# Performance work log

Hardware: AMD Instinct MI355X
Metric: run time of the kernel (lower is better)

## Reference

```python
import jax, jax.numpy as jnp
import numpy as np

N = 100000   # nodes
E = 1000000  # edges per scale
F = 500      # num_features
H = 64       # nhid
C = 40       # num_classes
S = 3        # scales = len(d_list) - 1


def setup_inputs() -> dict:
    key = jax.random.key(0)
    ks = jax.random.split(key, 24)
    inp = {}
    inp["x"] = jax.random.normal(ks[0], (N, F), jnp.float32)
    for i in range(S):
        inp[f"edge_index_{i+1}"] = jax.random.randint(ks[1 + i], (2, E), 0, N, dtype=jnp.int32)
        inp[f"edge_attr_{i+1}"] = jax.random.uniform(ks[4 + i], (E,), jnp.float32)
    # linear1: num_features -> nhid
    inp["W1"] = jax.random.normal(ks[7], (F, H), jnp.float32) * (1.0 / np.sqrt(F))
    inp["b1"] = jnp.zeros((H,), jnp.float32)
    # UFG filters, block 1 and block 2: uniform(0.7*i, 0.7*i + 0.1), shape [1, H]
    for i in range(S):
        lo = 0.7 * (i + 1)
        inp[f"filt1_{i+1}"] = jax.random.uniform(ks[8 + i], (1, H), jnp.float32, lo, lo + 0.1)
        inp[f"filt2_{i+1}"] = jax.random.uniform(ks[11 + i], (1, H), jnp.float32, lo, lo + 0.1)
    # mlp2: Linear(3*H, H) (after ReLU+Dropout)
    inp["W_mlp2"] = jax.random.normal(ks[14], (3 * H, H), jnp.float32) * (1.0 / np.sqrt(3 * H))
    inp["b_mlp2"] = jnp.zeros((H,), jnp.float32)
    # mlp1: Linear(3*H, C)
    inp["W_mlp1"] = jax.random.normal(ks[15], (3 * H, C), jnp.float32) * (1.0 / np.sqrt(3 * H))
    inp["b_mlp1"] = jnp.zeros((C,), jnp.float32)
    return inp


def _ufg(x, edge_index, edge_attr, filt):
    # MessagePassing(aggr='add'): out[dst] = sum_e attr_e * x[src_e]; then * filter
    src, dst = edge_index[0], edge_index[1]
    msg = edge_attr[:, None] * x[src]                       # [E, H]
    agg = jax.ops.segment_sum(msg, dst, num_segments=N)     # [N, H]
    return agg * filt


def reference(x, edge_index_1, edge_attr_1, edge_index_2, edge_attr_2,
              edge_index_3, edge_attr_3, W1, b1,
              filt1_1, filt1_2, filt1_3, filt2_1, filt2_2, filt2_3,
              W_mlp2, b_mlp2, W_mlp1, b_mlp1):
    eis = (edge_index_1, edge_index_2, edge_index_3)
    eas = (edge_attr_1, edge_attr_2, edge_attr_3)
    f1 = (filt1_1, filt1_2, filt1_3)
    f2 = (filt2_1, filt2_2, filt2_3)

    h = x @ W1 + b1                                          # [N, H]
    h = jnp.concatenate([_ufg(h, ei, ea, f) for ei, ea, f in zip(eis, eas, f1)], axis=1)  # [N, 3H]
    h = jax.nn.relu(h) @ W_mlp2 + b_mlp2                     # mlp2 (dropout = identity in eval)
    h = jnp.concatenate([_ufg(h, ei, ea, f) for ei, ea, f in zip(eis, eas, f2)], axis=1)  # [N, 3H]
    h = jax.nn.relu(h) @ W_mlp1 + b_mlp1                     # mlp1
    return jax.nn.log_softmax(h, axis=1)
```

## Files before the change

### kernel.cpp

```cpp
#include <hip/hip_runtime.h>
#include <hip/hip_bf16.h>

#define NN 100000
#define FF 500
#define HH 64
#define CC 40
#define EE 1000000
#define NB 782
#define NBK 2346
#define NBLK_P 256
#define M2 (NBK * NBLK_P)

typedef __attribute__((ext_vector_type(8))) short short8v;
typedef __attribute__((ext_vector_type(4))) float f32x4;

__device__ inline unsigned relu2bf16(unsigned u)
{
    unsigned r = (u & 0x00008000u) ? (u & 0xFFFF0000u) : u;
    return (r & 0x80000000u) ? (r & 0x0000FFFFu) : r;
}

__global__ __launch_bounds__(256) void build_w1t(
    const float* __restrict__ W1, __hip_bfloat16* __restrict__ W1t)
{
    int idx = blockIdx.x * 256 + threadIdx.x;
    if (idx >= 64 * 512) return;
    int col = idx >> 9;
    int k = idx & 511;
    W1t[idx] = (k < FF) ? __float2bfloat16(W1[(size_t)k * 64 + col])
                        : __float2bfloat16(0.f);
}

__global__ __launch_bounds__(256) void build_wm2t(
    const float* __restrict__ Wm2, __hip_bfloat16* __restrict__ Wm2t)
{
    int idx = blockIdx.x * 256 + threadIdx.x;
    if (idx >= 64 * 192) return;
    int col = idx / 192;
    int k = idx - col * 192;
    Wm2t[idx] = __float2bfloat16(Wm2[(size_t)k * 64 + col]);
}

__global__ __launch_bounds__(256) void gemm1_mfma(
    const float* __restrict__ X,
    const __hip_bfloat16* __restrict__ W1t,
    const float* __restrict__ bias,
    __hip_bfloat16* __restrict__ H,
    int nrows)
{
    __shared__ __hip_bfloat16 As[64][40];
    __shared__ __hip_bfloat16 Bs[64][40];

    const int t = threadIdx.x;
    const int lane = t & 63;
    const int w = t >> 6;
    const int row0 = blockIdx.x * 64;
    const int kg = lane >> 4;
    const int lr = lane & 15;

    f32x4 acc[4] = {};

    const int arow = t >> 2;
    const int akq = (t & 3) * 8;
    const int bcol = t >> 2;
    const int bkq = (t & 3) * 8;

    int grow = row0 + arow;
    const float* xp = X + (size_t)(grow < nrows ? grow : nrows - 1) * FF;

    float va[8];
    uint4 vb;
    {
        float4 a0 = *(const float4*)(xp + akq);
        float4 a1 = *(const float4*)(xp + akq + 4);
        va[0]=a0.x; va[1]=a0.y; va[2]=a0.z; va[3]=a0.w;
        va[4]=a1.x; va[5]=a1.y; va[6]=a1.z; va[7]=a1.w;
        vb = *(const uint4*)(W1t + (size_t)bcol * 512 + bkq);
    }

    for (int k0 = 0; k0 < FF; k0 += 32) {
        {
            unsigned q[4];
            #pragma unroll
            for (int i = 0; i < 4; ++i) {
                __hip_bfloat162 pp =
                    __float22bfloat162_rn(make_float2(va[2*i], va[2*i+1]));
                q[i] = *(unsigned*)&pp;
            }
            *(uint4*)&As[arow][akq] = make_uint4(q[0], q[1], q[2], q[3]);
            *(uint4*)&Bs[bcol][bkq] = vb;
        }

        const int kn = k0 + 32;
        float va2[8];
        uint4 vb2;
        if (kn < FF) {
            if (kn + 32 <= FF) {
                float4 a0 = *(const float4*)(xp + kn + akq);
                float4 a1 = *(const float4*)(xp + kn + akq + 4);
                va2[0]=a0.x; va2[1]=a0.y; va2[2]=a0.z; va2[3]=a0.w;
                va2[4]=a1.x; va2[5]=a1.y; va2[6]=a1.z; va2[7]=a1.w;
            } else {
                #pragma unroll
                for (int j = 0; j < 8; ++j) {
                    int kk = kn + akq + j;
                    va2[j] = (kk < FF) ? xp[kk] : 0.f;
                }
            }
            vb2 = *(const uint4*)(W1t + (size_t)bcol * 512 + kn + bkq);
        }
        __syncthreads();

        short8v a0 = *(const short8v*)&As[w * 16 + lr][kg * 8];
        short8v b0 = *(const short8v*)&Bs[lr][kg * 8];
        short8v b1 = *(const short8v*)&Bs[16 + lr][kg * 8];
        short8v b2 = *(const short8v*)&Bs[32 + lr][kg * 8];
        short8v b3 = *(const short8v*)&Bs[48 + lr][kg * 8];
        acc[0] = __builtin_amdgcn_mfma_f32_16x16x32_bf16(a0, b0, acc[0], 0, 0, 0);
        acc[1] = __builtin_amdgcn_mfma_f32_16x16x32_bf16(a0, b1, acc[1], 0, 0, 0);
        acc[2] = __builtin_amdgcn_mfma_f32_16x16x32_bf16(a0, b2, acc[2], 0, 0, 0);
        acc[3] = __builtin_amdgcn_mfma_f32_16x16x32_bf16(a0, b3, acc[3], 0, 0, 0);
        __syncthreads();

        if (kn < FF) {
            #pragma unroll
            for (int j = 0; j < 8; ++j) va[j] = va2[j];
            vb = vb2;
        }
    }

    float bv[4];
    #pragma unroll
    for (int n = 0; n < 4; ++n) bv[n] = bias[n * 16 + lr];

    #pragma unroll
    for (int n = 0; n < 4; ++n) {
        #pragma unroll
        for (int r = 0; r < 4; ++r) {
            int row = row0 + w * 16 + kg * 4 + r;
            if (row < nrows)
                H[(size_t)row * 64 + n * 16 + lr] =
                    __float2bfloat16(acc[n][r] + bv[n]);
        }
    }
}

__global__ __launch_bounds__(256) void gemm2_mfma(
    const __hip_bfloat16* __restrict__ A,
    const __hip_bfloat16* __restrict__ Bt,
    const float* __restrict__ bias,
    __hip_bfloat16* __restrict__ H,
    int nrows)
{
    __shared__ __hip_bfloat16 As[128][40];
    __shared__ __hip_bfloat16 Bs[64][40];

    const int t = threadIdx.x;
    const int lane = t & 63;
    const int w = t >> 6;
    const int row0 = blockIdx.x * 128;
    const int wrow = w * 32;
    const int kg = lane >> 4;
    const int lr = lane & 15;

    f32x4 acc[2][4] = {};

    const int arow = t >> 1;
    const int akh = t & 1;
    const int bcol = t >> 2;
    const int bkq = t & 3;

    for (int k0 = 0; k0 < 192; k0 += 32) {
        {
            int grow = row0 + arow;
            int gr = grow < nrows ? grow : nrows - 1;
            const __hip_bfloat16* ap = A + (size_t)gr * 192 + k0 + akh * 16;
            uint4 u0 = *(const uint4*)ap;
            uint4 u1 = *(const uint4*)(ap + 8);
            u0.x = relu2bf16(u0.x); u0.y = relu2bf16(u0.y);
            u0.z = relu2bf16(u0.z); u0.w = relu2bf16(u0.w);
            u1.x = relu2bf16(u1.x); u1.y = relu2bf16(u1.y);
            u1.z = relu2bf16(u1.z); u1.w = relu2bf16(u1.w);
            *(uint4*)&As[arow][akh * 16]     = u0;
            *(uint4*)&As[arow][akh * 16 + 8] = u1;
        }
        *(uint4*)&Bs[bcol][bkq * 8] =
            *(const uint4*)(Bt + (size_t)bcol * 192 + k0 + bkq * 8);
        __syncthreads();

        short8v a0 = *(const short8v*)&As[wrow + lr][kg * 8];
        short8v a1 = *(const short8v*)&As[wrow + 16 + lr][kg * 8];
        short8v b0 = *(const short8v*)&Bs[lr][kg * 8];
        short8v b1 = *(const short8v*)&Bs[16 + lr][kg * 8];
        short8v b2 = *(const short8v*)&Bs[32 + lr][kg * 8];
        short8v b3 = *(const short8v*)&Bs[48 + lr][kg * 8];
        acc[0][0] = __builtin_amdgcn_mfma_f32_16x16x32_bf16(a0, b0, acc[0][0], 0, 0, 0);
        acc[0][1] = __builtin_amdgcn_mfma_f32_16x16x32_bf16(a0, b1, acc[0][1], 0, 0, 0);
        acc[0][2] = __builtin_amdgcn_mfma_f32_16x16x32_bf16(a0, b2, acc[0][2], 0, 0, 0);
        acc[0][3] = __builtin_amdgcn_mfma_f32_16x16x32_bf16(a0, b3, acc[0][3], 0, 0, 0);
        acc[1][0] = __builtin_amdgcn_mfma_f32_16x16x32_bf16(a1, b0, acc[1][0], 0, 0, 0);
        acc[1][1] = __builtin_amdgcn_mfma_f32_16x16x32_bf16(a1, b1, acc[1][1], 0, 0, 0);
        acc[1][2] = __builtin_amdgcn_mfma_f32_16x16x32_bf16(a1, b2, acc[1][2], 0, 0, 0);
        acc[1][3] = __builtin_amdgcn_mfma_f32_16x16x32_bf16(a1, b3, acc[1][3], 0, 0, 0);
        __syncthreads();
    }

    float bv[4];
    #pragma unroll
    for (int n = 0; n < 4; ++n) bv[n] = bias[n * 16 + lr];

    #pragma unroll
    for (int m = 0; m < 2; ++m) {
        #pragma unroll
        for (int n = 0; n < 4; ++n) {
            #pragma unroll
            for (int r = 0; r < 4; ++r) {
                int row = row0 + wrow + m * 16 + kg * 4 + r;
                if (row < nrows)
                    H[(size_t)row * 64 + n * 16 + lr] =
                        __float2bfloat16(acc[m][n][r] + bv[n]);
            }
        }
    }
}

__global__ __launch_bounds__(1024) void part_count(
    const int* __restrict__ ei1, const int* __restrict__ ei2,
    const int* __restrict__ ei3, int* __restrict__ cnt)
{
    __shared__ int lc[NBK];
    const int t = threadIdx.x;
    for (int j = t; j < NBK; j += 1024) lc[j] = 0;
    __syncthreads();

    const int chunk = (3 * EE + NBLK_P - 1) / NBLK_P;
    const int b0 = blockIdx.x * chunk;
    int b1 = b0 + chunk;
    if (b1 > 3 * EE) b1 = 3 * EE;

    for (int i = b0 + t; i < b1; i += 1024) {
        int s = i / EE;
        int e = i - s * EE;
        const int* ei = (s == 0) ? ei1 : (s == 1) ? ei2 : ei3;
        atomicAdd(&lc[s * NB + (ei[EE + e] >> 7)], 1);
    }
    __syncthreads();
    for (int j = t; j < NBK; j += 1024)
        cnt[j * NBLK_P + blockIdx.x] = lc[j];
}

__global__ __launch_bounds__(1024) void scan_a(
    const int* __restrict__ cnt, int* __restrict__ off,
    int* __restrict__ partials, int M)
{
    __shared__ int sh[1024];
    int t = threadIdx.x;
    int i = blockIdx.x * 1024 + t;
    int v = (i < M) ? cnt[i] : 0;
    sh[t] = v;
    __syncthreads();
    #pragma unroll
    for (int o = 1; o < 1024; o <<= 1) {
        int add = (t >= o) ? sh[t - o] : 0;
        __syncthreads();
        sh[t] += add;
        __syncthreads();
    }
    if (i < M) off[i] = sh[t] - v;
    if (t == 1023) partials[blockIdx.x] = sh[1023];
}

__global__ __launch_bounds__(1024) void scan_b(int* __restrict__ partials, int P)
{
    __shared__ int sh[1024];
    int t = threadIdx.x;
    int v = (t < P) ? partials[t] : 0;
    sh[t] = v;
    __syncthreads();
    #pragma unroll
    for (int o = 1; o < 1024; o <<= 1) {
        int add = (t >= o) ? sh[t - o] : 0;
        __syncthreads();
        sh[t] += add;
        __syncthreads();
    }
    if (t < P) partials[t] = sh[t] - v;
}

__global__ __launch_bounds__(256) void scan_c(
    int* __restrict__ off, int* __restrict__ off_b,
    const int* __restrict__ partials, int M)
{
    int i = blockIdx.x * 256 + threadIdx.x;
    if (i < M) {
        int v = off[i] + partials[i >> 10];
        off[i] = v;
        if ((i & (NBLK_P - 1)) == 0) off_b[i / NBLK_P] = v;
    }
    if (i == 0) off_b[NBK] = 3 * EE;
}

__global__ __launch_bounds__(1024) void part_scatter(
    const int* __restrict__ ei1, const float* __restrict__ ea1,
    const int* __restrict__ ei2, const float* __restrict__ ea2,
    const int* __restrict__ ei3, const float* __restrict__ ea3,
    const int* __restrict__ offp, int2* __restrict__ brec)
{
    __shared__ int lcur[NBK];
    const int t = threadIdx.x;
    for (int j = t; j < NBK; j += 1024)
        lcur[j] = offp[j * NBLK_P + blockIdx.x];
    __syncthreads();

    const int chunk = (3 * EE + NBLK_P - 1) / NBLK_P;
    const int b0 = blockIdx.x * chunk;
    int b1 = b0 + chunk;
    if (b1 > 3 * EE) b1 = 3 * EE;

    for (int i = b0 + t; i < b1; i += 1024) {
        int s = i / EE;
        int e = i - s * EE;
        const int* ei = (s == 0) ? ei1 : (s == 1) ? ei2 : ei3;
        const float* ea = (s == 0) ? ea1 : (s == 1) ? ea2 : ea3;
        int src = ei[e];
        int dst = ei[EE + e];
        float w = ea[e];
        int pos = atomicAdd(&lcur[s * NB + (dst >> 7)], 1);
        brec[pos] = make_int2(src | ((dst & 127) << 17), __float_as_int(w));
    }
}

__global__ __launch_bounds__(256) void bucket_refine(
    const int2* __restrict__ brec,
    const int* __restrict__ off_b,
    int* __restrict__ node_off,
    int2* __restrict__ pairs)
{
    __shared__ int hist[128];
    __shared__ int curls[128];
    const int t = threadIdx.x;
    const int bk = blockIdx.x;
    const int s = bk / NB;
    const int b = bk - s * NB;
    const int n0 = b << 7;
    const int beg = off_b[bk];
    const int end = off_b[bk + 1];

    if (bk == 0 && t == 0) node_off[3 * NN] = 3 * EE;
    if (t < 128) hist[t] = 0;
    __syncthreads();

    for (int p = beg + t; p < end; p += 256)
        atomicAdd(&hist[(brec[p].x >> 17) & 127], 1);
    __syncthreads();

    int cnt = (t < 128) ? hist[t] : 0;
    #pragma unroll
    for (int o = 1; o < 128; o <<= 1) {
        int add = (t < 128 && t >= o) ? hist[t - o] : 0;
        __syncthreads();
        if (t < 128) hist[t] += add;
        __syncthreads();
    }
    if (t < 128) {
        int excl = beg + hist[t] - cnt;
        curls[t] = excl;
        if (n0 + t < NN) node_off[s * NN + n0 + t] = excl;
    }
    __syncthreads();

    for (int p = beg + t; p < end; p += 256) {
        int2 r = brec[p];
        int pos = atomicAdd(&curls[(r.x >> 17) & 127], 1);
        pairs[pos] = make_int2(r.x & 0x1FFFF, r.y);
    }
}

__device__ inline void drain_seg(
    const __hip_bfloat16* __restrict__ h, const int2* __restrict__ pairs,
    unsigned lane, int p, int end, float& acc0, float& acc1)
{
    for (; p + 8 <= end; p += 8) {
        int2 q[8];
        #pragma unroll
        for (int i = 0; i < 8; ++i) q[i] = pairs[p + i];
        float v[8];
        #pragma unroll
        for (int i = 0; i < 8; ++i)
            v[i] = __bfloat162float(h[((unsigned)q[i].x << 6) | lane]);
        #pragma unroll
        for (int i = 0; i < 8; i += 2) {
            acc0 = fmaf(__int_as_float(q[i].y), v[i], acc0);
            acc1 = fmaf(__int_as_float(q[i + 1].y), v[i + 1], acc1);
        }
    }
    if (p + 4 <= end) {
        int2 q[4];
        #pragma unroll
        for (int i = 0; i < 4; ++i) q[i] = pairs[p + i];
        float v[4];
        #pragma unroll
        for (int i = 0; i < 4; ++i)
            v[i] = __bfloat162float(h[((unsigned)q[i].x << 6) | lane]);
        acc0 = fmaf(__int_as_float(q[0].y), v[0], acc0);
        acc1 = fmaf(__int_as_float(q[1].y), v[1], acc1);
        acc0 = fmaf(__int_as_float(q[2].y), v[2], acc0);
        acc1 = fmaf(__int_as_float(q[3].y), v[3], acc1);
        p += 4;
    }
    if (p + 2 <= end) {
        int2 q0 = pairs[p];
        int2 q1 = pairs[p + 1];
        float v0 = __bfloat162float(h[((unsigned)q0.x << 6) | lane]);
        float v1 = __bfloat162float(h[((unsigned)q1.x << 6) | lane]);
        acc0 = fmaf(__int_as_float(q0.y), v0, acc0);
        acc1 = fmaf(__int_as_float(q1.y), v1, acc1);
        p += 2;
    }
    if (p < end) {
        int2 q = pairs[p];
        acc0 = fmaf(__int_as_float(q.y),
                    __bfloat162float(h[((unsigned)q.x << 6) | lane]), acc0);
    }
}

__global__ __launch_bounds__(256) void ufg_gather(
    const __hip_bfloat16* __restrict__ h,
    const int* __restrict__ off,
    const int2* __restrict__ pairs,
    const float* __restrict__ f1, const float* __restrict__ f2,
    const float* __restrict__ f3,
    __hip_bfloat16* __restrict__ agg)
{
    const unsigned lane = threadIdx.x & 63;
    int wp0 = blockIdx.x * 4 + (threadIdx.x >> 6);
    const int wp = __builtin_amdgcn_readfirstlane(wp0);
    if (wp >= (3 * NN) / 2) return;
    const int segA = wp * 2;
    const int s = segA / NN;
    const int nA = segA - s * NN;

    const float* fp = (s == 0) ? f1 : (s == 1) ? f2 : f3;
    const float fv = fp[lane];

    const int begA = off[segA];
    const int endA = off[segA + 1];
    const int endB = off[segA + 2];

    float aA0 = 0.f, aA1 = 0.f, aB0 = 0.f, aB1 = 0.f;
    int pA = begA, pB = endA;

    while (pA + 8 <= endA && pB + 8 <= endB) {
        int2 qa[8], qb[8];
        #pragma unroll
        for (int i = 0; i < 8; ++i) qa[i] = pairs[pA + i];
        #pragma unroll
        for (int i = 0; i < 8; ++i) qb[i] = pairs[pB + i];
        float va[8], vb[8];
        #pragma unroll
        for (int i = 0; i < 8; ++i)
            va[i] = __bfloat162float(h[((unsigned)qa[i].x << 6) | lane]);
        #pragma unroll
        for (int i = 0; i < 8; ++i)
            vb[i] = __bfloat162float(h[((unsigned)qb[i].x << 6) | lane]);
        #pragma unroll
        for (int i = 0; i < 8; i += 2) {
            aA0 = fmaf(__int_as_float(qa[i].y), va[i], aA0);
            aA1 = fmaf(__int_as_float(qa[i + 1].y), va[i + 1], aA1);
            aB0 = fmaf(__int_as_float(qb[i].y), vb[i], aB0);
            aB1 = fmaf(__int_as_float(qb[i + 1].y), vb[i + 1], aB1);
        }
        pA += 8;
        pB += 8;
    }
    while (pA + 4 <= endA && pB + 4 <= endB) {
        int2 qa[4], qb[4];
        #pragma unroll
        for (int i = 0; i < 4; ++i) qa[i] = pairs[pA + i];
        #pragma unroll
        for (int i = 0; i < 4; ++i) qb[i] = pairs[pB + i];
        float va[4], vb[4];
        #pragma unroll
        for (int i = 0; i < 4; ++i)
            va[i] = __bfloat162float(h[((unsigned)qa[i].x << 6) | lane]);
        #pragma unroll
        for (int i = 0; i < 4; ++i)
            vb[i] = __bfloat162float(h[((unsigned)qb[i].x << 6) | lane]);
        aA0 = fmaf(__int_as_float(qa[0].y), va[0], aA0);
        aA1 = fmaf(__int_as_float(qa[1].y), va[1], aA1);
        aA0 = fmaf(__int_as_float(qa[2].y), va[2], aA0);
        aA1 = fmaf(__int_as_float(qa[3].y), va[3], aA1);
        aB0 = fmaf(__int_as_float(qb[0].y), vb[0], aB0);
        aB1 = fmaf(__int_as_float(qb[1].y), vb[1], aB1);
        aB0 = fmaf(__int_as_float(qb[2].y), vb[2], aB0);
        aB1 = fmaf(__int_as_float(qb[3].y), vb[3], aB1);
        pA += 4;
        pB += 4;
    }
    drain_seg(h, pairs, lane, pA, endA, aA0, aA1);
    drain_seg(h, pairs, lane, pB, endB, aB0, aB1);

    agg[(size_t)nA * 192 + s * 64 + lane] =
        __float2bfloat16((aA0 + aA1) * fv);
    agg[(size_t)(nA + 1) * 192 + s * 64 + lane] =
        __float2bfloat16((aB0 + aB1) * fv);
}

__global__ __launch_bounds__(256) void gemm40_softmax(
    const __hip_bfloat16* __restrict__ A,
    const float* __restrict__ B,
    const float* __restrict__ bias,
    float* __restrict__ out,
    int nrows)
{
    __shared__ float As[32][68];
    __shared__ float Bs[32][64];

    const int tid = threadIdx.x;
    const int tx = tid & 15;
    const int ty = tid >> 4;
    const int row0 = blockIdx.x * 64;

    float acc[4][4] = {{0.f, 0.f, 0.f, 0.f}, {0.f, 0.f, 0.f, 0.f},
                       {0.f, 0.f, 0.f, 0.f}, {0.f, 0.f, 0.f, 0.f}};

    const int r = tid >> 2;
    const int koff = (tid & 3) * 8;
    const bool rowok = (row0 + r) < nrows;

    for (int k0 = 0; k0 < 192; k0 += 32) {
        float av[8];
        const __hip_bfloat16* ap = A + (size_t)(row0 + r) * 192 + (k0 + koff);
        if (rowok) {
            uint4 u = *(const uint4*)ap;
            av[0] = __uint_as_float(u.x << 16);
            av[1] = __uint_as_float(u.x & 0xFFFF0000u);
            av[2] = __uint_as_float(u.y << 16);
            av[3] = __uint_as_float(u.y & 0xFFFF0000u);
            av[4] = __uint_as_float(u.z << 16);
            av[5] = __uint_as_float(u.z & 0xFFFF0000u);
            av[6] = __uint_as_float(u.w << 16);
            av[7] = __uint_as_float(u.w & 0xFFFF0000u);
        } else {
            #pragma unroll
            for (int j = 0; j < 8; ++j) av[j] = 0.f;
        }
        #pragma unroll
        for (int j = 0; j < 8; ++j) As[koff + j][r] = fmaxf(av[j], 0.f);

        {
            int flat = tid * 8;
            int kk = flat >> 6;
            int c0 = flat & 63;
            #pragma unroll
            for (int j = 0; j < 8; ++j) {
                int cc = c0 + j;
                Bs[kk][cc] = (cc < 40) ? B[(size_t)(k0 + kk) * 40 + cc] : 0.f;
            }
        }
        __syncthreads();

        #pragma unroll
        for (int k = 0; k < 32; ++k) {
            float4 a = *(const float4*)&As[k][ty * 4];
            float4 b = *(const float4*)&Bs[k][tx * 4];
            acc[0][0] = fmaf(a.x, b.x, acc[0][0]);
            acc[0][1] = fmaf(a.x, b.y, acc[0][1]);
            acc[0][2] = fmaf(a.x, b.z, acc[0][2]);
            acc[0][3] = fmaf(a.x, b.w, acc[0][3]);
            acc[1][0] = fmaf(a.y, b.x, acc[1][0]);
            acc[1][1] = fmaf(a.y, b.y, acc[1][1]);
            acc[1][2] = fmaf(a.y, b.z, acc[1][2]);
            acc[1][3] = fmaf(a.y, b.w, acc[1][3]);
            acc[2][0] = fmaf(a.z, b.x, acc[2][0]);
            acc[2][1] = fmaf(a.z, b.y, acc[2][1]);
            acc[2][2] = fmaf(a.z, b.z, acc[2][2]);
            acc[2][3] = fmaf(a.z, b.w, acc[2][3]);
            acc[3][0] = fmaf(a.w, b.x, acc[3][0]);
            acc[3][1] = fmaf(a.w, b.y, acc[3][1]);
            acc[3][2] = fmaf(a.w, b.z, acc[3][2]);
            acc[3][3] = fmaf(a.w, b.w, acc[3][3]);
        }
        __syncthreads();
    }

    float bv[4];
    #pragma unroll
    for (int j = 0; j < 4; ++j) {
        int cc = tx * 4 + j;
        bv[j] = (cc < 40) ? bias[cc] : 0.f;
    }
    const bool colok = (tx < 10);

    #pragma unroll
    for (int i = 0; i < 4; ++i) {
        float v0 = colok ? acc[i][0] + bv[0] : -1e30f;
        float v1 = colok ? acc[i][1] + bv[1] : -1e30f;
        float v2 = colok ? acc[i][2] + bv[2] : -1e30f;
        float v3 = colok ? acc[i][3] + bv[3] : -1e30f;

        float mx = fmaxf(fmaxf(v0, v1), fmaxf(v2, v3));
        #pragma unroll
        for (int o = 1; o < 16; o <<= 1)
            mx = fmaxf(mx, __shfl_xor(mx, o, 64));

        float s = __expf(v0 - mx) + __expf(v1 - mx) +
                  __expf(v2 - mx) + __expf(v3 - mx);
        #pragma unroll
        for (int o = 1; o < 16; o <<= 1)
            s += __shfl_xor(s, o, 64);

        int rr = row0 + ty * 4 + i;
        if (rr < nrows && colok) {
            float ls = mx + __logf(s);
            *(float4*)(out + (size_t)rr * 40 + tx * 4) =
                make_float4(v0 - ls, v1 - ls, v2 - ls, v3 - ls);
        }
    }
}

extern "C" void kernel_launch(void* const* d_in, const int* in_sizes, int n_in,
                              void* d_out, int out_size, void* d_ws, size_t ws_size,
                              hipStream_t stream)
{
    const float* x    = (const float*)d_in[0];
    const int*   ei1  = (const int*)d_in[1];
    const float* ea1  = (const float*)d_in[2];
    const int*   ei2  = (const int*)d_in[3];
    const float* ea2  = (const float*)d_in[4];
    const int*   ei3  = (const int*)d_in[5];
    const float* ea3  = (const float*)d_in[6];
    const float* W1   = (const float*)d_in[7];
    const float* b1   = (const float*)d_in[8];
    const float* f1_1 = (const float*)d_in[9];
    const float* f2_1 = (const float*)d_in[10];
    const float* f1_2 = (const float*)d_in[11];
    const float* f2_2 = (const float*)d_in[12];
    const float* f1_3 = (const float*)d_in[13];
    const float* f2_3 = (const float*)d_in[14];
    const float* Wm2  = (const float*)d_in[15];
    const float* bm2  = (const float*)d_in[16];
    const float* Wm1  = (const float*)d_in[17];
    const float* bm1  = (const float*)d_in[18];
    float* out = (float*)d_out;

    __hip_bfloat16* agg = (__hip_bfloat16*)d_ws;
    int2*  brec = (int2*)d_ws;
    char*  base = (char*)d_ws + (size_t)NN * 192 * 2;
    __hip_bfloat16* hbuf = (__hip_bfloat16*)base;
    int*   cnt  = (int*)(base + (size_t)NN * 64 * 2);
    int*   offp = cnt + M2;
    int*   part = offp + M2;
    int*   off_b = part + 1024;
    int*   node_off = off_b + NBK + 2;
    int2*  pairs = (int2*)(node_off + 3 * NN + 2);
    __hip_bfloat16* w1t = (__hip_bfloat16*)
        (((uintptr_t)(pairs + 3 * EE) + 15) & ~(uintptr_t)15);
    __hip_bfloat16* wm2t = w1t + 64 * 512;

    const int gemm_grid = (NN + 63) / 64;
    const int mfma2_grid = (NN + 127) / 128;
    const int gat_grid = ((3 * NN / 2) + 3) / 4;
    const int P = (M2 + 1023) / 1024;

    build_w1t<<<128, 256, 0, stream>>>(W1, w1t);
    build_wm2t<<<48, 256, 0, stream>>>(Wm2, wm2t);
    part_count<<<NBLK_P, 1024, 0, stream>>>(ei1, ei2, ei3, cnt);
    scan_a<<<P, 1024, 0, stream>>>(cnt, offp, part, M2);
    scan_b<<<1, 1024, 0, stream>>>(part, P);
    scan_c<<<(M2 + 255) / 256, 256, 0, stream>>>(offp, off_b, part, M2);
    part_scatter<<<NBLK_P, 1024, 0, stream>>>(ei1, ea1, ei2, ea2, ei3, ea3,
                                              offp, brec);
    bucket_refine<<<NBK, 256, 0, stream>>>(brec, off_b, node_off, pairs);

    gemm1_mfma<<<gemm_grid, 256, 0, stream>>>(x, w1t, b1, hbuf, NN);
    ufg_gather<<<gat_grid, 256, 0, stream>>>(hbuf, node_off, pairs,
                                             f1_1, f1_2, f1_3, agg);
    gemm2_mfma<<<mfma2_grid, 256, 0, stream>>>(agg, wm2t, bm2, hbuf, NN);

    ufg_gather<<<gat_grid, 256, 0, stream>>>(hbuf, node_off, pairs,
                                             f2_1, f2_2, f2_3, agg);
    gemm40_softmax<<<gemm_grid, 256, 0, stream>>>(agg, Wm1, bm1, out, NN);
}
```

Measured before the change: 364.8 us.

## Use MFMA for final GEMM+log-softmax and gather four segments per wavefront

Replaces the scalar-FMA final 192x40 GEMM with a bf16 MFMA kernel fed by a padded, transposed copy of W_mlp1, keeping the fused bias and log-softmax epilogue. The UFG gather kernel now has each wavefront process four consecutive destination nodes, interleaving their edge loads to expose more memory-level parallelism, with pairwise tail handling afterwards. Costs are an extra small weight-transpose launch, bf16 rounding of the last layer's weights, and higher register pressure in the gather.

New measurement: 332.8 us. 8.8% less time.

```diff
diff --git a/kernel.cpp b/kernel.cpp
--- a/kernel.cpp
+++ b/kernel.cpp
@@ -39,6 +39,17 @@
     int col = idx / 192;
     int k = idx - col * 192;
     Wm2t[idx] = __float2bfloat16(Wm2[(size_t)k * 64 + col]);
+}
+
+__global__ __launch_bounds__(256) void build_wm1t(
+    const float* __restrict__ Wm1, __hip_bfloat16* __restrict__ Wm1t)
+{
+    int idx = blockIdx.x * 256 + threadIdx.x;
+    if (idx >= 64 * 192) return;
+    int col = idx / 192;
+    int k = idx - col * 192;
+    Wm1t[idx] = (col < 40) ? __float2bfloat16(Wm1[(size_t)k * 40 + col])
+                           : __float2bfloat16(0.f);
 }
 
 __global__ __launch_bounds__(256) void gemm1_mfma(
@@ -224,6 +235,109 @@
     }
 }
 
+__global__ __launch_bounds__(256) void gemm3_mfma(
+    const __hip_bfloat16* __restrict__ A,
+    const __hip_bfloat16* __restrict__ Bt,
+    const float* __restrict__ bias,
+    float* __restrict__ out,
+    int nrows)
+{
+    __shared__ __hip_bfloat16 As[128][40];
+    __shared__ __hip_bfloat16 Bs[64][40];
+
+    const int t = threadIdx.x;
+    const int lane = t & 63;
+    const int w = t >> 6;
+    const int row0 = blockIdx.x * 128;
+    const int wrow = w * 32;
+    const int kg = lane >> 4;
+    const int lr = lane & 15;
+
+    f32x4 acc[2][4] = {};
+
+    const int arow = t >> 1;
+    const int akh = t & 1;
+    const int bcol = t >> 2;
+    const int bkq = t & 3;
+
+    for (int k0 = 0; k0 < 192; k0 += 32) {
+        {
+            int grow = row0 + arow;
+            int gr = grow < nrows ? grow : nrows - 1;
+            const __hip_bfloat16* ap = A + (size_t)gr * 192 + k0 + akh * 16;
+            uint4 u0 = *(const uint4*)ap;
+            uint4 u1 = *(const uint4*)(ap + 8);
+            u0.x = relu2bf16(u0.x); u0.y = relu2bf16(u0.y);
+            u0.z = relu2bf16(u0.z); u0.w = relu2bf16(u0.w);
+            u1.x = relu2bf16(u1.x); u1.y = relu2bf16(u1.y);
+            u1.z = relu2bf16(u1.z); u1.w = relu2bf16(u1.w);
+            *(uint4*)&As[arow][akh * 16]     = u0;
+            *(uint4*)&As[arow][akh * 16 + 8] = u1;
+        }
+        *(uint4*)&Bs[bcol][bkq * 8] =
+            *(const uint4*)(Bt + (size_t)bcol * 192 + k0 + bkq * 8);
+        __syncthreads();
+
+        short8v a0 = *(const short8v*)&As[wrow + lr][kg * 8];
+        short8v a1 = *(const short8v*)&As[wrow + 16 + lr][kg * 8];
+        short8v b0 = *(const short8v*)&Bs[lr][kg * 8];
+        short8v b1 = *(const short8v*)&Bs[16 + lr][kg * 8];
+        short8v b2 = *(const short8v*)&Bs[32 + lr][kg * 8];
+        short8v b3 = *(const short8v*)&Bs[48 + lr][kg * 8];
+        acc[0][0] = __builtin_amdgcn_mfma_f32_16x16x32_bf16(a0, b0, acc[0][0], 0, 0, 0);
+        acc[0][1] = __builtin_amdgcn_mfma_f32_16x16x32_bf16(a0, b1, acc[0][1], 0, 0, 0);
+        acc[0][2] = __builtin_amdgcn_mfma_f32_16x16x32_bf16(a0, b2, acc[0][2], 0, 0, 0);
+        acc[0][3] = __builtin_amdgcn_mfma_f32_16x16x32_bf16(a0, b3, acc[0][3], 0, 0, 0);
+        acc[1][0] = __builtin_amdgcn_mfma_f32_16x16x32_bf16(a1, b0, acc[1][0], 0, 0, 0);
+        acc[1][1] = __builtin_amdgcn_mfma_f32_16x16x32_bf16(a1, b1, acc[1][1], 0, 0, 0);
+        acc[1][2] = __builtin_amdgcn_mfma_f32_16x16x32_bf16(a1, b2, acc[1][2], 0, 0, 0);
+        acc[1][3] = __builtin_amdgcn_mfma_f32_16x16x32_bf16(a1, b3, acc[1][3], 0, 0, 0);
+        __syncthreads();
+    }
+
+    float bv[4];
+    bool vld[4];
+    #pragma unroll
+    for (int n = 0; n < 4; ++n) {
+        int col = n * 16 + lr;
+        vld[n] = col < 40;
+        bv[n] = vld[n] ? bias[col] : 0.f;
+    }
+
+    #pragma unroll
+    for (int m = 0; m < 2; ++m) {
+        #pragma unroll
+        for (int r = 0; r < 4; ++r) {
+            int row = row0 + wrow + m * 16 + kg * 4 + r;
+            float v[4];
+            #pragma unroll
+            for (int n = 0; n < 4; ++n)
+                v[n] = vld[n] ? acc[m][n][r] + bv[n] : -1e30f;
+
+            float mx = fmaxf(fmaxf(v[0], v[1]), fmaxf(v[2], v[3]));
+            #pragma unroll
+            for (int o = 1; o < 16; o <<= 1)
+                mx = fmaxf(mx, __shfl_xor(mx, o, 64));
+
+            float sum = 0.f;
+            #pragma unroll
+            for (int n = 0; n < 4; ++n)
+                sum += vld[n] ? __expf(v[n] - mx) : 0.f;
+            #pragma unroll
+            for (int o = 1; o < 16; o <<= 1)
+                sum += __shfl_xor(sum, o, 64);
+
+            if (row < nrows) {
+                float ls = mx + __logf(sum);
+                #pragma unroll
+                for (int n = 0; n < 4; ++n)
+                    if (vld[n])
+                        out[(size_t)row * 40 + n * 16 + lr] = v[n] - ls;
+            }
+        }
+    }
+}
+
 __global__ __launch_bounds__(1024) void part_count(
     const int* __restrict__ ei1, const int* __restrict__ ei2,
     const int* __restrict__ ei3, int* __restrict__ cnt)
@@ -376,103 +490,11 @@
     }
 }
 
-__device__ inline void drain_seg(
+__device__ inline void joint44(
     const __hip_bfloat16* __restrict__ h, const int2* __restrict__ pairs,
-    unsigned lane, int p, int end, float& acc0, float& acc1)
-{
-    for (; p + 8 <= end; p += 8) {
-        int2 q[8];
-        #pragma unroll
-        for (int i = 0; i < 8; ++i) q[i] = pairs[p + i];
-        float v[8];
-        #pragma unroll
-        for (int i = 0; i < 8; ++i)
-            v[i] = __bfloat162float(h[((unsigned)q[i].x << 6) | lane]);
-        #pragma unroll
-        for (int i = 0; i < 8; i += 2) {
-            acc0 = fmaf(__int_as_float(q[i].y), v[i], acc0);
-            acc1 = fmaf(__int_as_float(q[i + 1].y), v[i + 1], acc1);
-        }
-    }
-    if (p + 4 <= end) {
-        int2 q[4];
-        #pragma unroll
-        for (int i = 0; i < 4; ++i) q[i] = pairs[p + i];
-        float v[4];
-        #pragma unroll
-        for (int i = 0; i < 4; ++i)
-            v[i] = __bfloat162float(h[((unsigned)q[i].x << 6) | lane]);
-        acc0 = fmaf(__int_as_float(q[0].y), v[0], acc0);
-        acc1 = fmaf(__int_as_float(q[1].y), v[1], acc1);
-        acc0 = fmaf(__int_as_float(q[2].y), v[2], acc0);
-        acc1 = fmaf(__int_as_float(q[3].y), v[3], acc1);
-        p += 4;
-    }
-    if (p + 2 <= end) {
-        int2 q0 = pairs[p];
-        int2 q1 = pairs[p + 1];
-        float v0 = __bfloat162float(h[((unsigned)q0.x << 6) | lane]);
-        float v1 = __bfloat162float(h[((unsigned)q1.x << 6) | lane]);
-        acc0 = fmaf(__int_as_float(q0.y), v0, acc0);
-        acc1 = fmaf(__int_as_float(q1.y), v1, acc1);
-        p += 2;
-    }
-    if (p < end) {
-        int2 q = pairs[p];
-        acc0 = fmaf(__int_as_float(q.y),
-                    __bfloat162float(h[((unsigned)q.x << 6) | lane]), acc0);
-    }
-}
-
-__global__ __launch_bounds__(256) void ufg_gather(
-    const __hip_bfloat16* __restrict__ h,
-    const int* __restrict__ off,
-    const int2* __restrict__ pairs,
-    const float* __restrict__ f1, const float* __restrict__ f2,
-    const float* __restrict__ f3,
-    __hip_bfloat16* __restrict__ agg)
-{
-    const unsigned lane = threadIdx.x & 63;
-    int wp0 = blockIdx.x * 4 + (threadIdx.x >> 6);
-    const int wp = __builtin_amdgcn_readfirstlane(wp0);
-    if (wp >= (3 * NN) / 2) return;
-    const int segA = wp * 2;
-    const int s = segA / NN;
-    const int nA = segA - s * NN;
-
-    const float* fp = (s == 0) ? f1 : (s == 1) ? f2 : f3;
-    const float fv = fp[lane];
-
-    const int begA = off[segA];
-    const int endA = off[segA + 1];
-    const int endB = off[segA + 2];
-
-    float aA0 = 0.f, aA1 = 0.f, aB0 = 0.f, aB1 = 0.f;
-    int pA = begA, pB = endA;
-
-    while (pA + 8 <= endA && pB + 8 <= endB) {
-        int2 qa[8], qb[8];
-        #pragma unroll
-        for (int i = 0; i < 8; ++i) qa[i] = pairs[pA + i];
-        #pragma unroll
-        for (int i = 0; i < 8; ++i) qb[i] = pairs[pB + i];
-        float va[8], vb[8];
-        #pragma unroll
-        for (int i = 0; i < 8; ++i)
-            va[i] = __bfloat162float(h[((unsigned)qa[i].x << 6) | lane]);
-        #pragma unroll
-        for (int i = 0; i < 8; ++i)
-            vb[i] = __bfloat162float(h[((unsigned)qb[i].x << 6) | lane]);
-        #pragma unroll
-        for (int i = 0; i < 8; i += 2) {
-            aA0 = fmaf(__int_as_float(qa[i].y), va[i], aA0);
-            aA1 = fmaf(__int_as_float(qa[i + 1].y), va[i + 1], aA1);
-            aB0 = fmaf(__int_as_float(qb[i].y), vb[i], aB0);
-            aB1 = fmaf(__int_as_float(qb[i + 1].y), vb[i + 1], aB1);
-        }
-        pA += 8;
-        pB += 8;
-    }
+    unsigned lane, int& pA, int endA, int& pB, int endB,
+    float& aA0, float& aA1, float& aB0, float& aB1)
+{
     while (pA + 4 <= endA && pB + 4 <= endB) {
         int2 qa[4], qb[4];
         #pragma unroll
@@ -497,126 +519,130 @@
         pA += 4;
         pB += 4;
     }
-    drain_seg(h, pairs, lane, pA, endA, aA0, aA1);
-    drain_seg(h, pairs, lane, pB, endB, aB0, aB1);
-
-    agg[(size_t)nA * 192 + s * 64 + lane] =
-        __float2bfloat16((aA0 + aA1) * fv);
-    agg[(size_t)(nA + 1) * 192 + s * 64 + lane] =
-        __float2bfloat16((aB0 + aB1) * fv);
-}
-
-__global__ __launch_bounds__(256) void gemm40_softmax(
-    const __hip_bfloat16* __restrict__ A,
-    const float* __restrict__ B,
-    const float* __restrict__ bias,
-    float* __restrict__ out,
-    int nrows)
-{
-    __shared__ float As[32][68];
-    __shared__ float Bs[32][64];
-
-    const int tid = threadIdx.x;
-    const int tx = tid & 15;
-    const int ty = tid >> 4;
-    const int row0 = blockIdx.x * 64;
-
-    float acc[4][4] = {{0.f, 0.f, 0.f, 0.f}, {0.f, 0.f, 0.f, 0.f},
-                       {0.f, 0.f, 0.f, 0.f}, {0.f, 0.f, 0.f, 0.f}};
-
-    const int r = tid >> 2;
-    const int koff = (tid & 3) * 8;
-    const bool rowok = (row0 + r) < nrows;
-
-    for (int k0 = 0; k0 < 192; k0 += 32) {
-        float av[8];
-        const __hip_bfloat16* ap = A + (size_t)(row0 + r) * 192 + (k0 + koff);
-        if (rowok) {
-            uint4 u = *(const uint4*)ap;
-            av[0] = __uint_as_float(u.x << 16);
-            av[1] = __uint_as_float(u.x & 0xFFFF0000u);
-            av[2] = __uint_as_float(u.y << 16);
-            av[3] = __uint_as_float(u.y & 0xFFFF0000u);
-            av[4] = __uint_as_float(u.z << 16);
-            av[5] = __uint_as_float(u.z & 0xFFFF0000u);
-            av[6] = __uint_as_float(u.w << 16);
-            av[7] = __uint_as_float(u.w & 0xFFFF0000u);
-        } else {
-            #pragma unroll
-            for (int j = 0; j < 8; ++j) av[j] = 0.f;
-        }
-        #pragma unroll
-        for (int j = 0; j < 8; ++j) As[koff + j][r] = fmaxf(av[j], 0.f);
-
-        {
-            int flat = tid * 8;
-            int kk = flat >> 6;
-            int c0 = flat & 63;
-            #pragma unroll
-            for (int j = 0; j < 8; ++j) {
-                int cc = c0 + j;
-                Bs[kk][cc] = (cc < 40) ? B[(size_t)(k0 + kk) * 40 + cc] : 0.f;
-            }
-        }
-        __syncthreads();
-
-        #pragma unroll
-        for (int k = 0; k < 32; ++k) {
-            float4 a = *(const float4*)&As[k][ty * 4];
-            float4 b = *(const float4*)&Bs[k][tx * 4];
-            acc[0][0] = fmaf(a.x, b.x, acc[0][0]);
-            acc[0][1] = fmaf(a.x, b.y, acc[0][1]);
-            acc[0][2] = fmaf(a.x, b.z, acc[0][2]);
-            acc[0][3] = fmaf(a.x, b.w, acc[0][3]);
-            acc[1][0] = fmaf(a.y, b.x, acc[1][0]);
-            acc[1][1] = fmaf(a.y, b.y, acc[1][1]);
-            acc[1][2] = fmaf(a.y, b.z, acc[1][2]);
-            acc[1][3] = fmaf(a.y, b.w, acc[1][3]);
-            acc[2][0] = fmaf(a.z, b.x, acc[2][0]);
-            acc[2][1] = fmaf(a.z, b.y, acc[2][1]);
-            acc[2][2] = fmaf(a.z, b.z, acc[2][2]);
-            acc[2][3] = fmaf(a.z, b.w, acc[2][3]);
-            acc[3][0] = fmaf(a.w, b.x, acc[3][0]);
-            acc[3][1] = fmaf(a.w, b.y, acc[3][1]);
-            acc[3][2] = fmaf(a.w, b.z, acc[3][2]);
-            acc[3][3] = fmaf(a.w, b.w, acc[3][3]);
-        }
-        __syncthreads();
-    }
-
-    float bv[4];
-    #pragma unroll
-    for (int j = 0; j < 4; ++j) {
-        int cc = tx * 4 + j;
-        bv[j] = (cc < 40) ? bias[cc] : 0.f;
-    }
-    const bool colok = (tx < 10);
-
-    #pragma unroll
-    for (int i = 0; i < 4; ++i) {
-        float v0 = colok ? acc[i][0] + bv[0] : -1e30f;
-        float v1 = colok ? acc[i][1] + bv[1] : -1e30f;
-        float v2 = colok ? acc[i][2] + bv[2] : -1e30f;
-        float v3 = colok ? acc[i][3] + bv[3] : -1e30f;
-
-        float mx = fmaxf(fmaxf(v0, v1), fmaxf(v2, v3));
-        #pragma unroll
-        for (int o = 1; o < 16; o <<= 1)
-            mx = fmaxf(mx, __shfl_xor(mx, o, 64));
-
-        float s = __expf(v0 - mx) + __expf(v1 - mx) +
-                  __expf(v2 - mx) + __expf(v3 - mx);
-        #pragma unroll
-        for (int o = 1; o < 16; o <<= 1)
-            s += __shfl_xor(s, o, 64);
-
-        int rr = row0 + ty * 4 + i;
-        if (rr < nrows && colok) {
-            float ls = mx + __logf(s);
-            *(float4*)(out + (size_t)rr * 40 + tx * 4) =
-                make_float4(v0 - ls, v1 - ls, v2 - ls, v3 - ls);
-        }
-    }
+}
+
+__device__ inline void drain_seg(
+    const __hip_bfloat16* __restrict__ h, const int2* __restrict__ pairs,
+    unsigned lane, int p, int end, float& acc0, float& acc1)
+{
+    for (; p + 8 <= end; p += 8) {
+        int2 q[8];
+        #pragma unroll
+        for (int i = 0; i < 8; ++i) q[i] = pairs[p + i];
+        float v[8];
+        #pragma unroll
+        for (int i = 0; i < 8; ++i)
+            v[i] = __bfloat162float(h[((unsigned)q[i].x << 6) | lane]);
+        #pragma unroll
+        for (int i = 0; i < 8; i += 2) {
+            acc0 = fmaf(__int_as_float(q[i].y), v[i], acc0);
+            acc1 = fmaf(__int_as_float(q[i + 1].y), v[i + 1], acc1);
+        }
+    }
+    if (p + 4 <= end) {
+        int2 q[4];
+        #pragma unroll
+        for (int i = 0; i < 4; ++i) q[i] = pairs[p + i];
+        float v[4];
+        #pragma unroll
+        for (int i = 0; i < 4; ++i)
+            v[i] = __bfloat162float(h[((unsigned)q[i].x << 6) | lane]);
+        acc0 = fmaf(__int_as_float(q[0].y), v[0], acc0);
+        acc1 = fmaf(__int_as_float(q[1].y), v[1], acc1);
+        acc0 = fmaf(__int_as_float(q[2].y), v[2], acc0);
+        acc1 = fmaf(__int_as_float(q[3].y), v[3], acc1);
+        p += 4;
+    }
+    if (p + 2 <= end) {
+        int2 q0 = pairs[p];
+        int2 q1 = pairs[p + 1];
+        float v0 = __bfloat162float(h[((unsigned)q0.x << 6) | lane]);
+        float v1 = __bfloat162float(h[((unsigned)q1.x << 6) | lane]);
+        acc0 = fmaf(__int_as_float(q0.y), v0, acc0);
+        acc1 = fmaf(__int_as_float(q1.y), v1, acc1);
+        p += 2;
+    }
+    if (p < end) {
+        int2 q = pairs[p];
+        acc0 = fmaf(__int_as_float(q.y),
+                    __bfloat162float(h[((unsigned)q.x << 6) | lane]), acc0);
+    }
+}
+
+__global__ __launch_bounds__(256) void ufg_gather(
+    const __hip_bfloat16* __restrict__ h,
+    const int* __restrict__ off,
+    const int2* __restrict__ pairs,
+    const float* __restrict__ f1, const float* __restrict__ f2,
+    const float* __restrict__ f3,
+    __hip_bfloat16* __restrict__ agg)
+{
+    const unsigned lane = threadIdx.x & 63;
+    int wq0 = blockIdx.x * 4 + (threadIdx.x >> 6);
+    const int wq = __builtin_amdgcn_readfirstlane(wq0);
+    if (wq >= (3 * NN) / 4) return;
+    const int seg0 = wq * 4;
+    const int s = seg0 / NN;
+    const int n0 = seg0 - s * NN;
+
+    const float* fp = (s == 0) ? f1 : (s == 1) ? f2 : f3;
+    const float fv = fp[lane];
+
+    const int o0 = off[seg0];
+    const int o1 = off[seg0 + 1];
+    const int o2 = off[seg0 + 2];
+    const int o3 = off[seg0 + 3];
+    const int o4 = off[seg0 + 4];
+
+    float aA0 = 0.f, aA1 = 0.f, aB0 = 0.f, aB1 = 0.f;
+    float aC0 = 0.f, aC1 = 0.f, aD0 = 0.f, aD1 = 0.f;
+    int pA = o0, pB = o1, pC = o2, pD = o3;
+
+    while (pA + 4 <= o1 && pB + 4 <= o2 && pC + 4 <= o3 && pD + 4 <= o4) {
+        int2 q[16];
+        #pragma unroll
+        for (int i = 0; i < 4; ++i) {
+            q[i]      = pairs[pA + i];
+            q[4 + i]  = pairs[pB + i];
+            q[8 + i]  = pairs[pC + i];
+            q[12 + i] = pairs[pD + i];
+        }
+        float v[16];
+        #pragma unroll
+        for (int i = 0; i < 16; ++i)
+            v[i] = __bfloat162float(h[((unsigned)q[i].x << 6) | lane]);
+        aA0 = fmaf(__int_as_float(q[0].y),  v[0],  aA0);
+        aA1 = fmaf(__int_as_float(q[1].y),  v[1],  aA1);
+        aA0 = fmaf(__int_as_float(q[2].y),  v[2],  aA0);
+        aA1 = fmaf(__int_as_float(q[3].y),  v[3],  aA1);
+        aB0 = fmaf(__int_as_float(q[4].y),  v[4],  aB0);
+        aB1 = fmaf(__int_as_float(q[5].y),  v[5],  aB1);
+        aB0 = fmaf(__int_as_float(q[6].y),  v[6],  aB0);
+        aB1 = fmaf(__int_as_float(q[7].y),  v[7],  aB1);
+        aC0 = fmaf(__int_as_float(q[8].y),  v[8],  aC0);
+        aC1 = fmaf(__int_as_float(q[9].y),  v[9],  aC1);
+        aC0 = fmaf(__int_as_float(q[10].y), v[10], aC0);
+        aC1 = fmaf(__int_as_float(q[11].y), v[11], aC1);
+        aD0 = fmaf(__int_as_float(q[12].y), v[12], aD0);
+        aD1 = fmaf(__int_as_float(q[13].y), v[13], aD1);
+        aD0 = fmaf(__int_as_float(q[14].y), v[14], aD0);
+        aD1 = fmaf(__int_as_float(q[15].y), v[15], aD1);
+        pA += 4; pB += 4; pC += 4; pD += 4;
+    }
+    joint44(h, pairs, lane, pA, o1, pB, o2, aA0, aA1, aB0, aB1);
+    joint44(h, pairs, lane, pC, o3, pD, o4, aC0, aC1, aD0, aD1);
+    joint44(h, pairs, lane, pA, o1, pC, o3, aA0, aA1, aC0, aC1);
+    joint44(h, pairs, lane, pB, o2, pD, o4, aB0, aB1, aD0, aD1);
+    drain_seg(h, pairs, lane, pA, o1, aA0, aA1);
+    drain_seg(h, pairs, lane, pB, o2, aB0, aB1);
+    drain_seg(h, pairs, lane, pC, o3, aC0, aC1);
+    drain_seg(h, pairs, lane, pD, o4, aD0, aD1);
+
+    const size_t basei = (size_t)n0 * 192 + s * 64 + lane;
+    agg[basei]       = __float2bfloat16((aA0 + aA1) * fv);
+    agg[basei + 192] = __float2bfloat16((aB0 + aB1) * fv);
+    agg[basei + 384] = __float2bfloat16((aC0 + aC1) * fv);
+    agg[basei + 576] = __float2bfloat16((aD0 + aD1) * fv);
 }
 
 extern "C" void kernel_launch(void* const* d_in, const int* in_sizes, int n_in,
@@ -657,14 +683,16 @@
     __hip_bfloat16* w1t = (__hip_bfloat16*)
         (((uintptr_t)(pairs + 3 * EE) + 15) & ~(uintptr_t)15);
     __hip_bfloat16* wm2t = w1t + 64 * 512;
+    __hip_bfloat16* wm1t = wm2t + 64 * 192;
 
     const int gemm_grid = (NN + 63) / 64;
     const int mfma2_grid = (NN + 127) / 128;
-    const int gat_grid = ((3 * NN / 2) + 3) / 4;
+    const int gat_grid = ((3 * NN / 4) + 3) / 4;
     const int P = (M2 + 1023) / 1024;
 
     build_w1t<<<128, 256, 0, stream>>>(W1, w1t);
     build_wm2t<<<48, 256, 0, stream>>>(Wm2, wm2t);
+    build_wm1t<<<48, 256, 0, stream>>>(Wm1, wm1t);
     part_count<<<NBLK_P, 1024, 0, stream>>>(ei1, ei2, ei3, cnt);
     scan_a<<<P, 1024, 0, stream>>>(cnt, offp, part, M2);
     scan_b<<<1, 1024, 0, stream>>>(part, P);
@@ -680,5 +708,5 @@
 
     ufg_gather<<<gat_grid, 256, 0, stream>>>(hbuf, node_off, pairs,
                                              f2_1, f2_2, f2_3, agg);
-    gemm40_softmax<<<gemm_grid, 256, 0, stream>>>(agg, Wm1, bm1, out, NN);
-}
+    gemm3_mfma<<<mfma2_grid, 256, 0, stream>>>(agg, wm1t, bm1, out, NN);
+}
```
